# Kernel optimization log

Measured on AMD Instinct MI355X. Metric: run time of the kernel, lower is better.

## Reference

```python
import jax, jax.numpy as jnp
import numpy as np

EMBED_DIM = 1024
NUM_HEAD = 16
HEAD_DIM = EMBED_DIM // NUM_HEAD
SCALE = HEAD_DIM ** -0.5


def setup_inputs() -> dict:
    key = jax.random.key(0)
    ks = jax.random.split(key, 8)
    B, N, K, D = 2, 2048, 2048, EMBED_DIM
    s = D ** -0.5
    return {
        "x": jax.random.normal(ks[0], (B, N, D), jnp.float32),
        "ctx": jax.random.normal(ks[1], (B, K, D), jnp.float32),
        "Wq": jax.random.normal(ks[2], (D, D), jnp.float32) * s,
        "bq": jnp.zeros((D,), jnp.float32),
        "Wkv": jax.random.normal(ks[3], (D, 2 * D), jnp.float32) * s,
        "bkv": jnp.zeros((2 * D,), jnp.float32),
        "Wproj": jax.random.normal(ks[4], (D, D), jnp.float32) * s,
        "bproj": jnp.zeros((D,), jnp.float32),
    }


def reference(x, ctx, Wq, bq, Wkv, bkv, Wproj, bproj):
    B, N, D = x.shape
    K = ctx.shape[1]
    H, hd = NUM_HEAD, HEAD_DIM
    # Q projection -> [B, H, N, hd]
    q = (x @ Wq + bq).reshape(B, N, H, hd).transpose(0, 2, 1, 3)
    # KV projection -> k, v each [B, H, K, hd]
    kv = (ctx @ Wkv + bkv).reshape(B, K, 2, H, hd).transpose(2, 0, 3, 1, 4)
    k, v = kv[0], kv[1]
    # scaled dot-product attention with materialized scores [B, H, N, K]
    attn = jnp.einsum("bhnd,bhkd->bhnk", q * SCALE, k)
    attn = jax.nn.softmax(attn, axis=-1)
    out = jnp.einsum("bhnk,bhkd->bhnd", attn, v)
    out = out.transpose(0, 2, 1, 3).reshape(B, N, D)
    return out @ Wproj + bproj
```

## Files before the change

### kernel.cpp

```cpp
#include <hip/hip_runtime.h>
#include <hip/hip_bf16.h>

typedef __attribute__((ext_vector_type(8))) short bf16x8;
typedef __attribute__((ext_vector_type(4))) float f32x4;
typedef unsigned short u16;
typedef unsigned int u32;

#define NUM_HEAD 16
#define HEAD_DIM 64
#define SEQ_N 2048
#define SEQ_K 2048
#define EMB 1024
#define MROWS 4096
static constexpr float ATTN_SCALE_LOG2E = 0.125f * 1.44269504f;

#if __has_builtin(__builtin_amdgcn_exp2f)
#define EXP2(x) __builtin_amdgcn_exp2f(x)
#else
#define EXP2(x) __expf(0.69314718056f * (x))
#endif

__device__ __forceinline__ u16 f2bf(float f) {
  __hip_bfloat16 h = __float2bfloat16(f);
  return *reinterpret_cast<u16*>(&h);
}

__device__ __forceinline__ void async16(const u16* g, u16* l) {
  __builtin_amdgcn_global_load_lds(
      (const __attribute__((address_space(1))) unsigned int*)g,
      (__attribute__((address_space(3))) unsigned int*)l, 16, 0, 0);
}

__global__ __launch_bounds__(256) void cvt2(const float* __restrict__ x,
                                            const float* __restrict__ ctx,
                                            u16* __restrict__ xb, u16* __restrict__ cb) {
  const int n4 = MROWS * EMB / 4;
  int gid = blockIdx.x * 256 + threadIdx.x;
  const float4* s; ushort4* d; int i;
  if (gid < n4) { s = (const float4*)x;   d = (ushort4*)xb; i = gid; }
  else          { s = (const float4*)ctx; d = (ushort4*)cb; i = gid - n4; }
  float4 v = s[i];
  ushort4 o;
  o.x = f2bf(v.x); o.y = f2bf(v.y); o.z = f2bf(v.z); o.w = f2bf(v.w);
  d[i] = o;
}

__global__ __launch_bounds__(256) void transpose_cvt4(
    const float* __restrict__ Wq, const float* __restrict__ Wkv,
    const float* __restrict__ Wproj,
    u16* __restrict__ Wqt, u16* __restrict__ Wkvt, u16* __restrict__ Wpt) {
  __shared__ float tile[32][33];
  const int z = blockIdx.z;
  const float* W; u16* Wt; int srcN, colbase;
  if (z == 0)      { W = Wq;    Wt = Wqt;                          srcN = 1024; colbase = 0; }
  else if (z == 1) { W = Wkv;   Wt = Wkvt;                         srcN = 2048; colbase = 0; }
  else if (z == 2) { W = Wkv;   Wt = Wkvt + (size_t)1024 * 1024;   srcN = 2048; colbase = 1024; }
  else             { W = Wproj; Wt = Wpt;                          srcN = 1024; colbase = 0; }
  int n0 = blockIdx.x * 32, k0 = blockIdx.y * 32;
  int tx = threadIdx.x & 31, ty = threadIdx.x >> 5;
  #pragma unroll
  for (int i = ty; i < 32; i += 8)
    tile[i][tx] = W[(size_t)(k0 + i) * srcN + colbase + n0 + tx];
  __syncthreads();
  #pragma unroll
  for (int i = ty; i < 32; i += 8)
    Wt[(size_t)(n0 + i) * 1024 + k0 + tx] = f2bf(tile[tx][i]);
}

__global__ __launch_bounds__(256, 3) void gemm_qkv(
    const u16* __restrict__ xb, const u16* __restrict__ cb,
    const u16* __restrict__ Wqt, const u16* __restrict__ Wkvt,
    const float* __restrict__ bq, const float* __restrict__ bkv,
    u16* __restrict__ Qb, u16* __restrict__ Kb, u16* __restrict__ Vtb)
{
  __shared__ alignas(16) u16 smem[(64 + 256) * 64];
  u16* As = smem;
  u16* Bs = smem + 64 * 64;
  const int tid = threadIdx.x;
  const bool isQ = (blockIdx.y < 4);
  const int n0 = (isQ ? blockIdx.y : blockIdx.y - 4) * 256;
  const int m0 = blockIdx.x * 64;
  const u16* A      = isQ ? xb : cb;
  const u16* Wt     = isQ ? Wqt : Wkvt;
  const float* bias = isQ ? bq : bkv;
  const int wave = tid >> 6, lane = tid & 63;
  const int wm = (wave >> 1) * 32, wn = (wave & 1) * 128;
  const int l15 = lane & 15, quad = lane >> 4;

  f32x4 acc[2][8];
  #pragma unroll
  for (int i = 0; i < 2; i++)
    #pragma unroll
    for (int j = 0; j < 8; j++)
      #pragma unroll
      for (int r = 0; r < 4; r++) acc[i][j][r] = 0.0f;

  const int srow = tid >> 3;
  const int scol = (tid & 7) * 8;
  const u16* ag = A + (size_t)(m0 + srow) * EMB + scol;
  const u16* bg = Wt + (size_t)(n0 + srow) * EMB + scol;
  const int ldsoff = tid * 8;

  for (int kt = 0; kt < EMB; kt += 64) {
    #pragma unroll
    for (int s = 0; s < 2; s++)
      async16(ag + (size_t)(s * 32) * EMB + kt, &As[ldsoff + s * 2048]);
    #pragma unroll
    for (int s = 0; s < 8; s++)
      async16(bg + (size_t)(s * 32) * EMB + kt, &Bs[ldsoff + s * 2048]);
    __syncthreads();
    #pragma unroll
    for (int ks = 0; ks < 2; ks++) {
      bf16x8 af[2], bfr[8];
      #pragma unroll
      for (int i = 0; i < 2; i++)
        af[i]  = *(const bf16x8*)&As[(wm + i * 16 + l15) * 64 + ks * 32 + quad * 8];
      #pragma unroll
      for (int j = 0; j < 8; j++)
        bfr[j] = *(const bf16x8*)&Bs[(wn + j * 16 + l15) * 64 + ks * 32 + quad * 8];
      #pragma unroll
      for (int i = 0; i < 2; i++)
        #pragma unroll
        for (int j = 0; j < 8; j++)
          acc[i][j] = __builtin_amdgcn_mfma_f32_16x16x32_bf16(af[i], bfr[j], acc[i][j], 0, 0, 0);
    }
    __syncthreads();
  }

  if (isQ) {
    #pragma unroll
    for (int i = 0; i < 2; i++) {
      #pragma unroll
      for (int j = 0; j < 8; j++) {
        const int gc = n0 + wn + j * 16 + l15;
        const float bv = bias[gc];
        const int h = gc >> 6, d = gc & 63;
        #pragma unroll
        for (int r = 0; r < 4; r++) {
          const int gm = m0 + wm + i * 16 + quad * 4 + r;
          const int bb = gm >> 11, nn = gm & 2047;
          Qb[((size_t)(bb * NUM_HEAD + h) * SEQ_N + nn) * HEAD_DIM + d] =
              f2bf((acc[i][j][r] + bv) * ATTN_SCALE_LOG2E);
        }
      }
    }
  } else {
    const int s = n0 >> 10;
    if (s == 0) {
      #pragma unroll
      for (int i = 0; i < 2; i++) {
        #pragma unroll
        for (int j = 0; j < 8; j++) {
          const int gc = n0 + wn + j * 16 + l15;
          const float bv = bias[gc];
          const int h = gc >> 6, d = gc & 63;
          #pragma unroll
          for (int r = 0; r < 4; r++) {
            const int gm = m0 + wm + i * 16 + quad * 4 + r;
            const int bb = gm >> 11, kk = gm & 2047;
            Kb[((size_t)(bb * NUM_HEAD + h) * SEQ_K + kk) * HEAD_DIM + d] =
                f2bf(acc[i][j][r] + bv);
          }
        }
      }
    } else {
      u16* wbuf = smem + wave * 1280;
      const int gm0 = m0 + wm;
      const int bb = gm0 >> 11;
      const int kk0 = gm0 & 2047;
      const int hbase = ((n0 + wn) >> 6) & 15;
      #pragma unroll
      for (int hh2 = 0; hh2 < 2; hh2++) {
        #pragma unroll
        for (int p = 0; p < 2; p++) {
          #pragma unroll
          for (int jj = 0; jj < 2; jj++) {
            const int j = hh2 * 4 + p * 2 + jj;
            const int gc = n0 + wn + j * 16 + l15;
            const float bv = bias[gc];
            #pragma unroll
            for (int i = 0; i < 2; i++) {
              ushort4 pk;
              pk.x = f2bf(acc[i][j][0] + bv);
              pk.y = f2bf(acc[i][j][1] + bv);
              pk.z = f2bf(acc[i][j][2] + bv);
              pk.w = f2bf(acc[i][j][3] + bv);
              *(ushort4*)&wbuf[(jj * 16 + l15) * 40 + i * 16 + quad * 4] = pk;
            }
          }
          __syncthreads();
          u32* dstu = (u32*)(Vtb +
              ((size_t)(bb * NUM_HEAD + hbase + hh2) * HEAD_DIM + p * 32) * SEQ_K + kk0);
          #pragma unroll
          for (int it = 0; it < 8; it++) {
            const int dd = it * 4 + quad;
            const int kp = l15 * 2;
            u32 v = *(const u32*)&wbuf[dd * 40 + kp];
            dstu[(size_t)dd * (SEQ_K / 2) + (kp >> 1)] = v;
          }
          __syncthreads();
        }
      }
    }
  }
}

__global__ __launch_bounds__(256) void gemm_proj(
    const u16* __restrict__ A, const u16* __restrict__ Wt,
    const float* __restrict__ bias, float* __restrict__ outF)
{
  __shared__ alignas(16) u16 smem[(64 + 128) * 64];
  u16* As = smem;
  u16* Bs = smem + 64 * 64;
  const int tid = threadIdx.x;
  const int n0 = blockIdx.y * 128, m0 = blockIdx.x * 64;
  const int wave = tid >> 6, lane = tid & 63;
  const int wm = (wave >> 1) * 32, wn = (wave & 1) * 64;
  const int l15 = lane & 15, quad = lane >> 4;

  f32x4 acc[2][4];
  #pragma unroll
  for (int i = 0; i < 2; i++)
    #pragma unroll
    for (int j = 0; j < 4; j++)
      #pragma unroll
      for (int r = 0; r < 4; r++) acc[i][j][r] = 0.0f;

  const int srow = tid >> 3;
  const int scol = (tid & 7) * 8;
  const u16* ag = A + (size_t)(m0 + srow) * EMB + scol;
  const u16* bg = Wt + (size_t)(n0 + srow) * EMB + scol;
  const int ldsoff = tid * 8;

  for (int kt = 0; kt < EMB; kt += 64) {
    async16(ag + kt, &As[ldsoff]);
    async16(ag + (size_t)32 * EMB + kt, &As[ldsoff + 2048]);
    #pragma unroll
    for (int s = 0; s < 4; s++)
      async16(bg + (size_t)(s * 32) * EMB + kt, &Bs[ldsoff + s * 2048]);
    __syncthreads();
    #pragma unroll
    for (int ks = 0; ks < 2; ks++) {
      bf16x8 af[2], bfr[4];
      #pragma unroll
      for (int i = 0; i < 2; i++)
        af[i]  = *(const bf16x8*)&As[(wm + i * 16 + l15) * 64 + ks * 32 + quad * 8];
      #pragma unroll
      for (int j = 0; j < 4; j++)
        bfr[j] = *(const bf16x8*)&Bs[(wn + j * 16 + l15) * 64 + ks * 32 + quad * 8];
      #pragma unroll
      for (int i = 0; i < 2; i++)
        #pragma unroll
        for (int j = 0; j < 4; j++)
          acc[i][j] = __builtin_amdgcn_mfma_f32_16x16x32_bf16(af[i], bfr[j], acc[i][j], 0, 0, 0);
    }
    __syncthreads();
  }

  #pragma unroll
  for (int i = 0; i < 2; i++) {
    #pragma unroll
    for (int j = 0; j < 4; j++) {
      const int gc = n0 + wn + j * 16 + l15;
      const float bv = bias[gc];
      #pragma unroll
      for (int r = 0; r < 4; r++) {
        const int gm = m0 + wm + i * 16 + quad * 4 + r;
        outF[(size_t)gm * EMB + gc] = acc[i][j][r] + bv;
      }
    }
  }
}

__global__ __launch_bounds__(256) void attn_kernel(
    const u16* __restrict__ Qb, const u16* __restrict__ Kb,
    const u16* __restrict__ Vtb, u16* __restrict__ Ob)
{
  __shared__ alignas(16) u16 Ks[64 * 72];
  __shared__ alignas(16) u16 Vs[64 * 72];
  __shared__ alignas(16) u16 Ps[4 * 32 * 72];
  const int tid = threadIdx.x;
  const int bh = blockIdx.x;
  const int m0 = blockIdx.y * 128;
  const int wave = tid >> 6, lane = tid & 63;
  const int l15 = lane & 15, quad = lane >> 4;
  const int rowb = m0 + wave * 32;

  bf16x8 bq[2][2];
  #pragma unroll
  for (int rs = 0; rs < 2; rs++) {
    const u16* qp = Qb + ((size_t)bh * SEQ_N + rowb + rs * 16 + l15) * HEAD_DIM + quad * 8;
    bq[rs][0] = *(const bf16x8*)(qp);
    bq[rs][1] = *(const bf16x8*)(qp + 32);
  }

  f32x4 o[2][4];
  #pragma unroll
  for (int rs = 0; rs < 2; rs++)
    #pragma unroll
    for (int dt = 0; dt < 4; dt++)
      #pragma unroll
      for (int r = 0; r < 4; r++) o[rs][dt][r] = 0.0f;
  float l_part[2] = {0.f, 0.f};
  u16* pbuf = Ps + wave * 32 * 72;

  const int kr = tid >> 3;
  const int ko = (tid & 7) * 8;
  const u16* kg = Kb + ((size_t)bh * SEQ_K + kr) * HEAD_DIM + ko;
  const u16* vg = Vtb + ((size_t)bh * HEAD_DIM + kr) * SEQ_K + ko;

  uint4 kA = *(const uint4*)(kg);
  uint4 kB = *(const uint4*)(kg + (size_t)32 * HEAD_DIM);
  uint4 vA = *(const uint4*)(vg);
  uint4 vB = *(const uint4*)(vg + (size_t)32 * SEQ_K);

  for (int kt = 0; kt < SEQ_K; kt += 64) {
    *(uint4*)&Ks[kr * 72 + ko]        = kA;
    *(uint4*)&Ks[(kr + 32) * 72 + ko] = kB;
    *(uint4*)&Vs[kr * 72 + ko]        = vA;
    *(uint4*)&Vs[(kr + 32) * 72 + ko] = vB;
    __syncthreads();

    if (kt + 64 < SEQ_K) {
      kA = *(const uint4*)(kg + (size_t)(kt + 64) * HEAD_DIM);
      kB = *(const uint4*)(kg + (size_t)(kt + 96) * HEAD_DIM);
      vA = *(const uint4*)(vg + kt + 64);
      vB = *(const uint4*)(vg + (size_t)32 * SEQ_K + kt + 64);
    }

    #pragma unroll
    for (int kt4 = 0; kt4 < 4; kt4++) {
      const bf16x8 a0 = *(const bf16x8*)&Ks[(kt4 * 16 + l15) * 72 + quad * 8];
      const bf16x8 a1 = *(const bf16x8*)&Ks[(kt4 * 16 + l15) * 72 + 32 + quad * 8];
      #pragma unroll
      for (int rs = 0; rs < 2; rs++) {
        f32x4 z = {0.f, 0.f, 0.f, 0.f};
        z = __builtin_amdgcn_mfma_f32_16x16x32_bf16(a0, bq[rs][0], z, 0, 0, 0);
        z = __builtin_amdgcn_mfma_f32_16x16x32_bf16(a1, bq[rs][1], z, 0, 0, 0);
        ushort4 pk;
        float p0 = EXP2(z[0]), p1 = EXP2(z[1]);
        float p2 = EXP2(z[2]), p3 = EXP2(z[3]);
        l_part[rs] += (p0 + p1) + (p2 + p3);
        pk.x = f2bf(p0); pk.y = f2bf(p1); pk.z = f2bf(p2); pk.w = f2bf(p3);
        *(ushort4*)&pbuf[(rs * 16 + l15) * 72 + kt4 * 16 + quad * 4] = pk;
      }
    }

    bf16x8 ap[2][2];
    #pragma unroll
    for (int rs = 0; rs < 2; rs++) {
      ap[rs][0] = *(const bf16x8*)&pbuf[(rs * 16 + l15) * 72 + quad * 8];
      ap[rs][1] = *(const bf16x8*)&pbuf[(rs * 16 + l15) * 72 + 32 + quad * 8];
    }
    #pragma unroll
    for (int dt = 0; dt < 4; dt++) {
      const bf16x8 v0 = *(const bf16x8*)&Vs[(dt * 16 + l15) * 72 + quad * 8];
      const bf16x8 v1 = *(const bf16x8*)&Vs[(dt * 16 + l15) * 72 + 32 + quad * 8];
      #pragma unroll
      for (int rs = 0; rs < 2; rs++) {
        o[rs][dt] = __builtin_amdgcn_mfma_f32_16x16x32_bf16(ap[rs][0], v0, o[rs][dt], 0, 0, 0);
        o[rs][dt] = __builtin_amdgcn_mfma_f32_16x16x32_bf16(ap[rs][1], v1, o[rs][dt], 0, 0, 0);
      }
    }
    __syncthreads();
  }

  float lsum[2];
  #pragma unroll
  for (int rs = 0; rs < 2; rs++) {
    float s = l_part[rs];
    s += __shfl_xor(s, 16, 64);
    s += __shfl_xor(s, 32, 64);
    lsum[rs] = s;
  }

  const int bb = bh >> 4, hh = bh & 15;
  #pragma unroll
  for (int rs = 0; rs < 2; rs++) {
    #pragma unroll
    for (int r = 0; r < 4; r++) {
      const float lv = __shfl(lsum[rs], quad * 4 + r, 64);
      const float inv = 1.0f / lv;
      const int gm = rowb + rs * 16 + quad * 4 + r;
      u16* op = Ob + ((size_t)bb * SEQ_N + gm) * EMB + hh * HEAD_DIM;
      #pragma unroll
      for (int dt = 0; dt < 4; dt++)
        op[dt * 16 + l15] = f2bf(o[rs][dt][r] * inv);
    }
  }
}

extern "C" void kernel_launch(void* const* d_in, const int* in_sizes, int n_in,
                              void* d_out, int out_size, void* d_ws, size_t ws_size,
                              hipStream_t stream)
{
  const float* x     = (const float*)d_in[0];
  const float* ctx   = (const float*)d_in[1];
  const float* Wq    = (const float*)d_in[2];
  const float* bq    = (const float*)d_in[3];
  const float* Wkv   = (const float*)d_in[4];
  const float* bkv   = (const float*)d_in[5];
  const float* Wproj = (const float*)d_in[6];
  const float* bproj = (const float*)d_in[7];
  float* out = (float*)d_out;

  char* ws = (char*)d_ws;
  size_t off = 0;
  auto walloc = [&](size_t bytes) -> void* {
    void* p = ws + off;
    off += (bytes + 255) & ~(size_t)255;
    return p;
  };
  u16* xb   = (u16*)walloc((size_t)MROWS * EMB * 2);
  u16* cb   = (u16*)walloc((size_t)MROWS * EMB * 2);
  u16* Wqt  = (u16*)walloc((size_t)EMB * EMB * 2);
  u16* Wkvt = (u16*)walloc((size_t)2 * EMB * EMB * 2);
  u16* Wpt  = (u16*)walloc((size_t)EMB * EMB * 2);
  u16* Qb   = (u16*)walloc((size_t)MROWS * EMB * 2);
  u16* Kb   = (u16*)walloc((size_t)MROWS * EMB * 2);
  u16* Vtb  = (u16*)walloc((size_t)MROWS * EMB * 2);
  u16* Ob   = (u16*)walloc((size_t)MROWS * EMB * 2);

  cvt2<<<8192, 256, 0, stream>>>(x, ctx, xb, cb);
  transpose_cvt4<<<dim3(32, 32, 4), 256, 0, stream>>>(Wq, Wkv, Wproj, Wqt, Wkvt, Wpt);
  gemm_qkv<<<dim3(64, 12), 256, 0, stream>>>(xb, cb, Wqt, Wkvt, bq, bkv, Qb, Kb, Vtb);
  attn_kernel<<<dim3(32, 16), 256, 0, stream>>>(Qb, Kb, Vtb, Ob);
  gemm_proj<<<dim3(64, 8), 256, 0, stream>>>(Ob, Wpt, bproj, out);
}
```

Before: 218.5 us.

## Double-buffer K/V tiles with async global-to-LDS loads and XOR swizzle

Replaces the register-staged K/V prefetch with direct asynchronous global-to-LDS copies into two ping-pong shared buffers. The next tile loads while the current one is consumed by the MFMAs. The padded 72-stride layout becomes an unpadded 64-stride layout with an XOR swizzle, to avoid bank conflicts on the fragment reads. This frees the registers that held the prefetched tile and removes the per-iteration store and barrier before compute. In exchange it doubles the LDS used for K/V and depends on the barrier to cover completion of the async copies.

```diff
diff --git a/kernel.cpp b/kernel.cpp
--- a/kernel.cpp
+++ b/kernel.cpp
@@ -276,8 +276,8 @@
     const u16* __restrict__ Qb, const u16* __restrict__ Kb,
     const u16* __restrict__ Vtb, u16* __restrict__ Ob)
 {
-  __shared__ alignas(16) u16 Ks[64 * 72];
-  __shared__ alignas(16) u16 Vs[64 * 72];
+  __shared__ alignas(16) u16 Ks[2][64 * 64];
+  __shared__ alignas(16) u16 Vs[2][64 * 64];
   __shared__ alignas(16) u16 Ps[4 * 32 * 72];
   const int tid = threadIdx.x;
   const int bh = blockIdx.x;
@@ -304,34 +304,34 @@
   float l_part[2] = {0.f, 0.f};
   u16* pbuf = Ps + wave * 32 * 72;
 
-  const int kr = tid >> 3;
-  const int ko = (tid & 7) * 8;
-  const u16* kg = Kb + ((size_t)bh * SEQ_K + kr) * HEAD_DIM + ko;
-  const u16* vg = Vtb + ((size_t)bh * HEAD_DIM + kr) * SEQ_K + ko;
-
-  uint4 kA = *(const uint4*)(kg);
-  uint4 kB = *(const uint4*)(kg + (size_t)32 * HEAD_DIM);
-  uint4 vA = *(const uint4*)(vg);
-  uint4 vB = *(const uint4*)(vg + (size_t)32 * SEQ_K);
+  const int srow = wave * 16 + (lane >> 3);
+  const int g2 = (((lane & 7) ^ (lane >> 3)) << 3);
+  const u16* kg = Kb + (size_t)bh * SEQ_K * HEAD_DIM;
+  const u16* vg = Vtb + (size_t)bh * HEAD_DIM * SEQ_K;
+  const int ldst = wave * 1024 + lane * 8;
+  const int swz = (l15 & 7) << 4;
+
+#define STAGE(kt_, nb_) do {                                               \
+    async16(kg + (size_t)((kt_) + srow) * HEAD_DIM + g2, &Ks[nb_][ldst]);       \
+    async16(kg + (size_t)((kt_) + srow + 8) * HEAD_DIM + g2, &Ks[nb_][ldst + 512]); \
+    async16(vg + (size_t)srow * SEQ_K + (kt_) + g2, &Vs[nb_][ldst]);            \
+    async16(vg + (size_t)(srow + 8) * SEQ_K + (kt_) + g2, &Vs[nb_][ldst + 512]); \
+  } while (0)
+
+  STAGE(0, 0);
+  __syncthreads();
 
   for (int kt = 0; kt < SEQ_K; kt += 64) {
-    *(uint4*)&Ks[kr * 72 + ko]        = kA;
-    *(uint4*)&Ks[(kr + 32) * 72 + ko] = kB;
-    *(uint4*)&Vs[kr * 72 + ko]        = vA;
-    *(uint4*)&Vs[(kr + 32) * 72 + ko] = vB;
-    __syncthreads();
-
-    if (kt + 64 < SEQ_K) {
-      kA = *(const uint4*)(kg + (size_t)(kt + 64) * HEAD_DIM);
-      kB = *(const uint4*)(kg + (size_t)(kt + 96) * HEAD_DIM);
-      vA = *(const uint4*)(vg + kt + 64);
-      vB = *(const uint4*)(vg + (size_t)32 * SEQ_K + kt + 64);
-    }
+    const int cur = (kt >> 6) & 1;
+    if (kt + 64 < SEQ_K) STAGE(kt + 64, cur ^ 1);
+    const char* KsB = (const char*)Ks[cur];
+    const char* VsB = (const char*)Vs[cur];
 
     #pragma unroll
     for (int kt4 = 0; kt4 < 4; kt4++) {
-      const bf16x8 a0 = *(const bf16x8*)&Ks[(kt4 * 16 + l15) * 72 + quad * 8];
-      const bf16x8 a1 = *(const bf16x8*)&Ks[(kt4 * 16 + l15) * 72 + 32 + quad * 8];
+      const int rb = (kt4 * 16 + l15) * 128;
+      const bf16x8 a0 = *(const bf16x8*)(KsB + rb + ((quad * 16) ^ swz));
+      const bf16x8 a1 = *(const bf16x8*)(KsB + rb + ((64 + quad * 16) ^ swz));
       #pragma unroll
       for (int rs = 0; rs < 2; rs++) {
         f32x4 z = {0.f, 0.f, 0.f, 0.f};
@@ -354,8 +354,9 @@
     }
     #pragma unroll
     for (int dt = 0; dt < 4; dt++) {
-      const bf16x8 v0 = *(const bf16x8*)&Vs[(dt * 16 + l15) * 72 + quad * 8];
-      const bf16x8 v1 = *(const bf16x8*)&Vs[(dt * 16 + l15) * 72 + 32 + quad * 8];
+      const int rb = (dt * 16 + l15) * 128;
+      const bf16x8 v0 = *(const bf16x8*)(VsB + rb + ((quad * 16) ^ swz));
+      const bf16x8 v1 = *(const bf16x8*)(VsB + rb + ((64 + quad * 16) ^ swz));
       #pragma unroll
       for (int rs = 0; rs < 2; rs++) {
         o[rs][dt] = __builtin_amdgcn_mfma_f32_16x16x32_bf16(ap[rs][0], v0, o[rs][dt], 0, 0, 0);
@@ -364,6 +365,7 @@
     }
     __syncthreads();
   }
+#undef STAGE
 
   float lsum[2];
   #pragma unroll
```

New measurement: 216.9 us. No clear change (-0.7%).
